# Kernel optimization log

Measured on AMD Instinct MI355X. Metric: run time of the kernel, lower is better.

## Reference

```python
import jax, jax.numpy as jnp
import numpy as np

EMB = 1024
HEADS = 16
RATE = 1.0


def setup_inputs() -> dict:
    key = jax.random.key(0)
    ks = jax.random.split(key, 11)
    B, S, D = 2, 2048, EMB
    s = 1.0 / np.sqrt(D)
    inp = {
        "q": jax.random.normal(ks[0], (B, S, D), jnp.float32),
        "k": jax.random.normal(ks[1], (B, S, D), jnp.float32),
        "v": jax.random.normal(ks[2], (B, S, D), jnp.float32),
        "Wq": jax.random.normal(ks[3], (D, D), jnp.float32) * s,
        "bq": jnp.zeros((D,), jnp.float32),
        "Wk": jax.random.normal(ks[4], (D, D), jnp.float32) * s,
        "bk": jnp.zeros((D,), jnp.float32),
        "Wv": jax.random.normal(ks[5], (D, D), jnp.float32) * s,
        "bv": jnp.zeros((D,), jnp.float32),
        "Wo": jax.random.normal(ks[6], (D, D), jnp.float32) * s,
        "bo": jnp.zeros((D,), jnp.float32),
    }
    return inp


def _mha(q, k, v, Wq, bq, Wk, bk, Wv, bv, Wo, bo):
    B, S, D = q.shape
    H = HEADS
    hd = D // H
    temp = jnp.asarray(hd ** 0.5, q.dtype)

    def proj(x, W, b):
        # nn.Linear: x @ W.T + b, then Scaler: /rate
        y = (jnp.einsum('bsd,ed->bse', x, W) + b) / RATE
        # [B,S,D] -> [B,H,S,hd]
        return y.reshape(B, S, H, hd).transpose(0, 2, 1, 3)

    qh, kh, vh = proj(q, Wq, bq), proj(k, Wk, bk), proj(v, Wv, bv)
    scores = jnp.einsum('bhqd,bhkd->bhqk', qh, kh) / temp  # [B,H,S,S]
    causal = jnp.tril(jnp.ones((S, S), bool))
    scores = jnp.where(causal, scores, jnp.asarray(-jnp.inf, scores.dtype))
    attn = jax.nn.softmax(scores, axis=-1)
    out = jnp.einsum('bhqk,bhkd->bhqd', attn, vh)  # [B,H,S,hd]
    out = out.transpose(0, 2, 1, 3).reshape(B, S, D)
    out = (jnp.einsum('bsd,ed->bse', out, Wo) + bo) / RATE
    # attn returned as [B*H, S, S] to match torch reshape-to-batches layout
    return out, attn.reshape(B * H, S, S)


def reference(q, k, v, Wq, bq, Wk, bk, Wv, bv, Wo, bo):
    return _mha(q, k, v, Wq, bq, Wk, bk, Wv, bv, Wo, bo)
```

## Files before the change

### kernel.cpp

```cpp
#include <hip/hip_runtime.h>
#include <hip/hip_bf16.h>
#include <stdint.h>


#define SLEN 2048
#define DMODEL 1024
#define NBH 32

typedef __bf16 bf16x8 __attribute__((ext_vector_type(8)));
typedef float f32x4 __attribute__((ext_vector_type(4)));
typedef unsigned short us8 __attribute__((ext_vector_type(8)));

__device__ __forceinline__ unsigned short f2bf(float f) {
  union { float f; uint32_t u; } x; x.f = f;
  uint32_t r = x.u + 0x7fffu + ((x.u >> 16) & 1u);
  return (unsigned short)(r >> 16);
}

__device__ __forceinline__ f32x4 mfma16(us8 a, us8 b, f32x4 c) {
  return __builtin_amdgcn_mfma_f32_16x16x32_bf16(
      __builtin_bit_cast(bf16x8, a), __builtin_bit_cast(bf16x8, b), c, 0, 0, 0);
}

__device__ __forceinline__ int sw8(int r, int c)  { return (r * 8  + (c ^ (r & 7)))  * 16; }
__device__ __forceinline__ int sw16(int r, int c) { return (r * 16 + (c ^ (r & 15))) * 16; }

__global__ __launch_bounds__(256)
void gemm_qkv(const float* __restrict__ xq, const float* __restrict__ xk,
              const float* __restrict__ xv, const float* __restrict__ wwq,
              const float* __restrict__ wwk, const float* __restrict__ wwv,
              const float* __restrict__ bbq, const float* __restrict__ bbk,
              const float* __restrict__ bbv,
              unsigned short* __restrict__ qh, unsigned short* __restrict__ kk,
              unsigned short* __restrict__ vt) {
  __shared__ __align__(16) unsigned char As[16384];
  __shared__ __align__(16) unsigned char Bs[16384];
  const int p = blockIdx.z;
  const float* X    = (p == 0) ? xq  : (p == 1) ? xk  : xv;
  const float* W    = (p == 0) ? wwq : (p == 1) ? wwk : wwv;
  const float* bias = (p == 0) ? bbq : (p == 1) ? bbk : bbv;
  const int n0 = blockIdx.x * 128, m0 = blockIdx.y * 128;
  const int t = threadIdx.x, lane = t & 63, w = t >> 6;
  const int quad = lane >> 4, l16 = lane & 15;
  const int wm = w >> 1, wn = w & 1;
  f32x4 acc[4][4] = {};

  for (int kt = 0; kt < 16; ++kt) {
#pragma unroll
    for (int i = 0; i < 4; ++i) {
      int lin = i * 256 + t;
      int r = lin >> 3, cp = lin & 7, c = cp ^ (r & 7);
      const float* g = X + (size_t)(m0 + r) * DMODEL + kt * 64 + c * 8;
      float4 f0 = *(const float4*)g;
      float4 f1 = *(const float4*)(g + 4);
      us8 u;
      u[0]=f2bf(f0.x); u[1]=f2bf(f0.y); u[2]=f2bf(f0.z); u[3]=f2bf(f0.w);
      u[4]=f2bf(f1.x); u[5]=f2bf(f1.y); u[6]=f2bf(f1.z); u[7]=f2bf(f1.w);
      *(us8*)(As + lin * 16) = u;
      const float* g2 = W + (size_t)(n0 + r) * DMODEL + kt * 64 + c * 8;
      float4 h0 = *(const float4*)g2;
      float4 h1 = *(const float4*)(g2 + 4);
      us8 vv;
      vv[0]=f2bf(h0.x); vv[1]=f2bf(h0.y); vv[2]=f2bf(h0.z); vv[3]=f2bf(h0.w);
      vv[4]=f2bf(h1.x); vv[5]=f2bf(h1.y); vv[6]=f2bf(h1.z); vv[7]=f2bf(h1.w);
      *(us8*)(Bs + lin * 16) = vv;
    }
    __syncthreads();
#pragma unroll
    for (int ks = 0; ks < 2; ++ks) {
      int c = ks * 4 + quad;
      us8 af[4], bf[4];
#pragma unroll
      for (int mt = 0; mt < 4; ++mt) af[mt] = *(const us8*)(As + sw8(wm * 64 + mt * 16 + l16, c));
#pragma unroll
      for (int nt = 0; nt < 4; ++nt) bf[nt] = *(const us8*)(Bs + sw8(wn * 64 + nt * 16 + l16, c));
#pragma unroll
      for (int mt = 0; mt < 4; ++mt)
#pragma unroll
        for (int nt = 0; nt < 4; ++nt)
          acc[mt][nt] = mfma16(af[mt], bf[nt], acc[mt][nt]);
    }
    __syncthreads();
  }
#pragma unroll
  for (int nt = 0; nt < 4; ++nt) {
    int e = n0 + wn * 64 + nt * 16 + l16;
    float bb = bias[e];
    int hh = e >> 6, tt = e & 63;
#pragma unroll
    for (int mt = 0; mt < 4; ++mt) {
#pragma unroll
      for (int rg = 0; rg < 4; ++rg) {
        int row = m0 + wm * 64 + mt * 16 + quad * 4 + rg;
        int b = row >> 11, s = row & 2047;
        unsigned short val = f2bf(acc[mt][nt][rg] + bb);
        int bhh = b * 16 + hh;
        if (p == 0)      qh[(size_t)(bhh * 2048 + s) * 64 + tt] = val;
        else if (p == 1) kk[(size_t)(bhh * 2048 + s) * 64 + tt] = val;
        else             vt[(size_t)(bhh * 64 + tt) * 2048 + s] = val;
      }
    }
  }
}

__global__ __launch_bounds__(256)
void attn_kernel(const unsigned short* __restrict__ qh,
                 const unsigned short* __restrict__ kk,
                 const unsigned short* __restrict__ vt,
                 unsigned short* __restrict__ ctx,
                 float* __restrict__ attn) {
  __shared__ __align__(16) unsigned char Ks[16384];
  __shared__ __align__(16) unsigned char Vts[16384];
  __shared__ __align__(16) unsigned char Ps[16384];
  const int bid = blockIdx.x;
  const int bh = bid >> 4;
  const int qt = (bid < 256) ? (bid & 15) : (15 - (bid & 15));
  const int q0 = qt * 128;
  const int t = threadIdx.x, lane = t & 63, w = t >> 6;
  const int quad = lane >> 4, l16 = lane & 15;
  const size_t bho = (size_t)bh * SLEN * 64;

  us8 qf[2][2];
#pragma unroll
  for (int mq = 0; mq < 2; ++mq)
#pragma unroll
    for (int ks = 0; ks < 2; ++ks)
      qf[mq][ks] = *(const us8*)(qh + bho + (size_t)(q0 + w * 32 + mq * 16 + l16) * 64 + ks * 32 + quad * 8);

  float mrow[2][4], lrow[2][4];
#pragma unroll
  for (int mq = 0; mq < 2; ++mq)
#pragma unroll
    for (int rg = 0; rg < 4; ++rg) { mrow[mq][rg] = -3e38f; lrow[mq][rg] = 0.f; }

  for (int kt = 0; kt <= qt; ++kt) {
    __syncthreads();
#pragma unroll
    for (int i = 0; i < 4; ++i) {
      int lin = i * 256 + t, r = lin >> 3, cp = lin & 7, c = cp ^ (r & 7);
      *(us8*)(Ks + lin * 16) = *(const us8*)(kk + bho + (size_t)(kt * 128 + r) * 64 + c * 8);
    }
    __syncthreads();
    f32x4 sacc[2][8] = {};
#pragma unroll
    for (int ks = 0; ks < 2; ++ks) {
      int c = ks * 4 + quad;
      us8 bfr[8];
#pragma unroll
      for (int nk = 0; nk < 8; ++nk) bfr[nk] = *(const us8*)(Ks + sw8(nk * 16 + l16, c));
#pragma unroll
      for (int mq = 0; mq < 2; ++mq)
#pragma unroll
        for (int nk = 0; nk < 8; ++nk)
          sacc[mq][nk] = mfma16(qf[mq][ks], bfr[nk], sacc[mq][nk]);
    }
    const bool diag = (kt == qt);
#pragma unroll
    for (int mq = 0; mq < 2; ++mq)
#pragma unroll
      for (int rg = 0; rg < 4; ++rg) {
        int qrow = q0 + w * 32 + mq * 16 + quad * 4 + rg;
        float sv[8];
        float pm = -3e38f;
#pragma unroll
        for (int nk = 0; nk < 8; ++nk) {
          float vvv = sacc[mq][nk][rg] * 0.125f;
          if (diag && (kt * 128 + nk * 16 + l16) > qrow) vvv = -3e38f;
          sv[nk] = vvv;
          pm = fmaxf(pm, vvv);
        }
        pm = fmaxf(pm, __shfl_xor(pm, 1));
        pm = fmaxf(pm, __shfl_xor(pm, 2));
        pm = fmaxf(pm, __shfl_xor(pm, 4));
        pm = fmaxf(pm, __shfl_xor(pm, 8));
        float mn = fmaxf(mrow[mq][rg], pm);
        float ps = 0.f;
#pragma unroll
        for (int nk = 0; nk < 8; ++nk) ps += __expf(sv[nk] - mn);
        ps += __shfl_xor(ps, 1);
        ps += __shfl_xor(ps, 2);
        ps += __shfl_xor(ps, 4);
        ps += __shfl_xor(ps, 8);
        lrow[mq][rg] = lrow[mq][rg] * __expf(mrow[mq][rg] - mn) + ps;
        mrow[mq][rg] = mn;
      }
  }
  float rl[2][4];
#pragma unroll
  for (int mq = 0; mq < 2; ++mq)
#pragma unroll
    for (int rg = 0; rg < 4; ++rg) rl[mq][rg] = 1.0f / lrow[mq][rg];

  f32x4 oacc[2][4] = {};
  float* attnb = attn + (size_t)bh * SLEN * SLEN + (size_t)q0 * SLEN;
  for (int kt = 0; kt < 16; ++kt) {
    if (kt <= qt) {
      __syncthreads();
#pragma unroll
      for (int i = 0; i < 4; ++i) {
        int lin = i * 256 + t, r = lin >> 3, cp = lin & 7, c = cp ^ (r & 7);
        *(us8*)(Ks + lin * 16) = *(const us8*)(kk + bho + (size_t)(kt * 128 + r) * 64 + c * 8);
      }
#pragma unroll
      for (int i = 0; i < 4; ++i) {
        int lin = i * 256 + t, r = lin >> 4, cp = lin & 15, c = cp ^ (r & 15);
        *(us8*)(Vts + lin * 16) = *(const us8*)(vt + bho + (size_t)r * SLEN + kt * 128 + c * 8);
      }
      __syncthreads();
      f32x4 sacc[2][8] = {};
#pragma unroll
      for (int ks = 0; ks < 2; ++ks) {
        int c = ks * 4 + quad;
        us8 bfr[8];
#pragma unroll
        for (int nk = 0; nk < 8; ++nk) bfr[nk] = *(const us8*)(Ks + sw8(nk * 16 + l16, c));
#pragma unroll
        for (int mq = 0; mq < 2; ++mq)
#pragma unroll
          for (int nk = 0; nk < 8; ++nk)
            sacc[mq][nk] = mfma16(qf[mq][ks], bfr[nk], sacc[mq][nk]);
      }
      const bool diag = (kt == qt);
#pragma unroll
      for (int mq = 0; mq < 2; ++mq)
#pragma unroll
        for (int nk = 0; nk < 8; ++nk) {
          int col = kt * 128 + nk * 16 + l16;
#pragma unroll
          for (int rg = 0; rg < 4; ++rg) {
            int qrow = q0 + w * 32 + mq * 16 + quad * 4 + rg;
            float vvv = sacc[mq][nk][rg] * 0.125f;
            float p = __expf(vvv - mrow[mq][rg]) * rl[mq][rg];
            if (diag && col > qrow) p = 0.f;
            sacc[mq][nk][rg] = p;
            attnb[(size_t)(w * 32 + mq * 16 + quad * 4 + rg) * SLEN + col] = p;
          }
        }
#pragma unroll
      for (int kh2 = 0; kh2 < 2; ++kh2) {
#pragma unroll
        for (int mq = 0; mq < 2; ++mq)
#pragma unroll
          for (int nkk = 0; nkk < 4; ++nkk) {
            int nk = kh2 * 4 + nkk;
#pragma unroll
            for (int rg = 0; rg < 4; ++rg) {
              int pr = w * 32 + mq * 16 + quad * 4 + rg;
              int kl = nkk * 16 + l16;
              *(unsigned short*)(Ps + (pr * 8 + ((kl >> 3) ^ (pr & 7))) * 16 + (kl & 7) * 2)
                  = f2bf(sacc[mq][nk][rg]);
            }
          }
#pragma unroll
        for (int ks = 0; ks < 2; ++ks) {
          int ca = ks * 4 + quad;
          us8 pa[2];
#pragma unroll
          for (int mq = 0; mq < 2; ++mq)
            pa[mq] = *(const us8*)(Ps + sw8(w * 32 + mq * 16 + l16, ca));
          int cb = kh2 * 8 + ks * 4 + quad;
          us8 vb[4];
#pragma unroll
          for (int nd = 0; nd < 4; ++nd) vb[nd] = *(const us8*)(Vts + sw16(nd * 16 + l16, cb));
#pragma unroll
          for (int mq = 0; mq < 2; ++mq)
#pragma unroll
            for (int nd = 0; nd < 4; ++nd)
              oacc[mq][nd] = mfma16(pa[mq], vb[nd], oacc[mq][nd]);
        }
      }
    } else {
      float4 z = make_float4(0.f, 0.f, 0.f, 0.f);
#pragma unroll
      for (int i = 0; i < 16; ++i) {
        int idx = i * 256 + t, r = idx >> 5, c4 = idx & 31;
        *(float4*)(attnb + (size_t)r * SLEN + kt * 128 + c4 * 4) = z;
      }
    }
  }
  int b = bh >> 4, h = bh & 15;
#pragma unroll
  for (int mq = 0; mq < 2; ++mq)
#pragma unroll
    for (int nd = 0; nd < 4; ++nd)
#pragma unroll
      for (int rg = 0; rg < 4; ++rg) {
        int qrow = q0 + w * 32 + mq * 16 + quad * 4 + rg;
        int e = h * 64 + nd * 16 + l16;
        ctx[(size_t)(b * SLEN + qrow) * DMODEL + e] = f2bf(oacc[mq][nd][rg]);
      }
}

__global__ __launch_bounds__(256)
void gemm_out(const unsigned short* __restrict__ ctx, const float* __restrict__ wo,
              const float* __restrict__ bo, float* __restrict__ out) {
  __shared__ __align__(16) unsigned char As[16384];
  __shared__ __align__(16) unsigned char Bs[16384];
  const int n0 = blockIdx.x * 128, m0 = blockIdx.y * 128;
  const int t = threadIdx.x, lane = t & 63, w = t >> 6;
  const int quad = lane >> 4, l16 = lane & 15;
  const int wm = w >> 1, wn = w & 1;
  f32x4 acc[4][4] = {};

  for (int kt = 0; kt < 16; ++kt) {
#pragma unroll
    for (int i = 0; i < 4; ++i) {
      int lin = i * 256 + t;
      int r = lin >> 3, cp = lin & 7, c = cp ^ (r & 7);
      *(us8*)(As + lin * 16) = *(const us8*)(ctx + (size_t)(m0 + r) * DMODEL + kt * 64 + c * 8);
      const float* g2 = wo + (size_t)(n0 + r) * DMODEL + kt * 64 + c * 8;
      float4 h0 = *(const float4*)g2;
      float4 h1 = *(const float4*)(g2 + 4);
      us8 vv;
      vv[0]=f2bf(h0.x); vv[1]=f2bf(h0.y); vv[2]=f2bf(h0.z); vv[3]=f2bf(h0.w);
      vv[4]=f2bf(h1.x); vv[5]=f2bf(h1.y); vv[6]=f2bf(h1.z); vv[7]=f2bf(h1.w);
      *(us8*)(Bs + lin * 16) = vv;
    }
    __syncthreads();
#pragma unroll
    for (int ks = 0; ks < 2; ++ks) {
      int c = ks * 4 + quad;
      us8 af[4], bf[4];
#pragma unroll
      for (int mt = 0; mt < 4; ++mt) af[mt] = *(const us8*)(As + sw8(wm * 64 + mt * 16 + l16, c));
#pragma unroll
      for (int nt = 0; nt < 4; ++nt) bf[nt] = *(const us8*)(Bs + sw8(wn * 64 + nt * 16 + l16, c));
#pragma unroll
      for (int mt = 0; mt < 4; ++mt)
#pragma unroll
        for (int nt = 0; nt < 4; ++nt)
          acc[mt][nt] = mfma16(af[mt], bf[nt], acc[mt][nt]);
    }
    __syncthreads();
  }
#pragma unroll
  for (int nt = 0; nt < 4; ++nt) {
    int e = n0 + wn * 64 + nt * 16 + l16;
    float bb = bo[e];
#pragma unroll
    for (int mt = 0; mt < 4; ++mt)
#pragma unroll
      for (int rg = 0; rg < 4; ++rg) {
        int row = m0 + wm * 64 + mt * 16 + quad * 4 + rg;
        out[(size_t)row * DMODEL + e] = acc[mt][nt][rg] + bb;
      }
  }
}

extern "C" void kernel_launch(void* const* d_in, const int* in_sizes, int n_in,
                              void* d_out, int out_size, void* d_ws, size_t ws_size,
                              hipStream_t stream) {
  const float* q  = (const float*)d_in[0];
  const float* k  = (const float*)d_in[1];
  const float* v  = (const float*)d_in[2];
  const float* Wq = (const float*)d_in[3];
  const float* bq = (const float*)d_in[4];
  const float* Wk = (const float*)d_in[5];
  const float* bk = (const float*)d_in[6];
  const float* Wv = (const float*)d_in[7];
  const float* bv = (const float*)d_in[8];
  const float* Wo = (const float*)d_in[9];
  const float* bo = (const float*)d_in[10];
  float* out  = (float*)d_out;
  float* attn = out + (size_t)2 * SLEN * DMODEL;

  unsigned short* qh  = (unsigned short*)d_ws;
  unsigned short* kh  = qh + (size_t)4194304;
  unsigned short* vt  = kh + (size_t)4194304;
  unsigned short* ctx = vt + (size_t)4194304;

  gemm_qkv<<<dim3(8, 32, 3), 256, 0, stream>>>(q, k, v, Wq, Wk, Wv, bq, bk, bv, qh, kh, vt);
  attn_kernel<<<512, 256, 0, stream>>>(qh, kh, vt, ctx, attn);
  gemm_out<<<dim3(8, 32), 256, 0, stream>>>(ctx, Wo, bo, out);
}
```

Measured before the change: 874.2 us.

## Pre-convert inputs to bf16 and use direct global-to-LDS loads

Result: faster. 794.0 us (-9.2%).

```diff
diff --git a/kernel.cpp b/kernel.cpp
--- a/kernel.cpp
+++ b/kernel.cpp
@@ -22,17 +22,112 @@
       __builtin_bit_cast(bf16x8, a), __builtin_bit_cast(bf16x8, b), c, 0, 0, 0);
 }
 
+__device__ __forceinline__ void gld16(void* lds, const void* g) {
+  __builtin_amdgcn_global_load_lds(
+      (__attribute__((address_space(1))) void*)(g),
+      (__attribute__((address_space(3))) void*)(lds), 16, 0, 0);
+}
+
 __device__ __forceinline__ int sw8(int r, int c)  { return (r * 8  + (c ^ (r & 7)))  * 16; }
 __device__ __forceinline__ int sw16(int r, int c) { return (r * 16 + (c ^ (r & 15))) * 16; }
 
 __global__ __launch_bounds__(256)
-void gemm_qkv(const float* __restrict__ xq, const float* __restrict__ xk,
-              const float* __restrict__ xv, const float* __restrict__ wwq,
-              const float* __restrict__ wwk, const float* __restrict__ wwv,
-              const float* __restrict__ bbq, const float* __restrict__ bbk,
-              const float* __restrict__ bbv,
-              unsigned short* __restrict__ qh, unsigned short* __restrict__ kk,
-              unsigned short* __restrict__ vt) {
+void convert_bf16(const float* __restrict__ q, const float* __restrict__ k,
+                  const float* __restrict__ v, const float* __restrict__ wq,
+                  const float* __restrict__ wk, const float* __restrict__ wv,
+                  const float* __restrict__ wo, unsigned short* __restrict__ dst) {
+  size_t i = ((size_t)blockIdx.x * 256 + threadIdx.x) * 8;
+  const float* src;
+  size_t off;
+  if      (i <  4194304u) { src = q;  off = i; }
+  else if (i <  8388608u) { src = k;  off = i -  4194304u; }
+  else if (i < 12582912u) { src = v;  off = i -  8388608u; }
+  else if (i < 13631488u) { src = wq; off = i - 12582912u; }
+  else if (i < 14680064u) { src = wk; off = i - 13631488u; }
+  else if (i < 15728640u) { src = wv; off = i - 14680064u; }
+  else                    { src = wo; off = i - 15728640u; }
+  float4 a = *(const float4*)(src + off);
+  float4 b = *(const float4*)(src + off + 4);
+  us8 u;
+  u[0]=f2bf(a.x); u[1]=f2bf(a.y); u[2]=f2bf(a.z); u[3]=f2bf(a.w);
+  u[4]=f2bf(b.x); u[5]=f2bf(b.y); u[6]=f2bf(b.z); u[7]=f2bf(b.w);
+  *(us8*)(dst + i) = u;
+}
+
+__global__ __launch_bounds__(256)
+void gemm_qkv_bf(const unsigned short* __restrict__ xq, const unsigned short* __restrict__ xk,
+                 const unsigned short* __restrict__ xv, const unsigned short* __restrict__ wwq,
+                 const unsigned short* __restrict__ wwk, const unsigned short* __restrict__ wwv,
+                 const float* __restrict__ bbq, const float* __restrict__ bbk,
+                 const float* __restrict__ bbv,
+                 unsigned short* __restrict__ qh, unsigned short* __restrict__ kk,
+                 unsigned short* __restrict__ vt) {
+  __shared__ __align__(16) unsigned char As[16384];
+  __shared__ __align__(16) unsigned char Bs[16384];
+  const int p = blockIdx.z;
+  const unsigned short* X = (p == 0) ? xq  : (p == 1) ? xk  : xv;
+  const unsigned short* W = (p == 0) ? wwq : (p == 1) ? wwk : wwv;
+  const float* bias       = (p == 0) ? bbq : (p == 1) ? bbk : bbv;
+  const int n0 = blockIdx.x * 128, m0 = blockIdx.y * 128;
+  const int t = threadIdx.x, lane = t & 63, w = t >> 6;
+  const int quad = lane >> 4, l16 = lane & 15;
+  const int wm = w >> 1, wn = w & 1;
+  f32x4 acc[4][4] = {};
+
+  for (int kt = 0; kt < 16; ++kt) {
+#pragma unroll
+    for (int i = 0; i < 4; ++i) {
+      int lin = i * 256 + t;
+      int r = lin >> 3, cp = lin & 7, c = cp ^ (r & 7);
+      gld16(As + lin * 16, X + (size_t)(m0 + r) * DMODEL + kt * 64 + c * 8);
+      gld16(Bs + lin * 16, W + (size_t)(n0 + r) * DMODEL + kt * 64 + c * 8);
+    }
+    __syncthreads();
+#pragma unroll
+    for (int ks = 0; ks < 2; ++ks) {
+      int c = ks * 4 + quad;
+      us8 af[4], bf[4];
+#pragma unroll
+      for (int mt = 0; mt < 4; ++mt) af[mt] = *(const us8*)(As + sw8(wm * 64 + mt * 16 + l16, c));
+#pragma unroll
+      for (int nt = 0; nt < 4; ++nt) bf[nt] = *(const us8*)(Bs + sw8(wn * 64 + nt * 16 + l16, c));
+#pragma unroll
+      for (int mt = 0; mt < 4; ++mt)
+#pragma unroll
+        for (int nt = 0; nt < 4; ++nt)
+          acc[mt][nt] = mfma16(af[mt], bf[nt], acc[mt][nt]);
+    }
+    __syncthreads();
+  }
+#pragma unroll
+  for (int nt = 0; nt < 4; ++nt) {
+    int e = n0 + wn * 64 + nt * 16 + l16;
+    float bb = bias[e];
+    int hh = e >> 6, tt = e & 63;
+#pragma unroll
+    for (int mt = 0; mt < 4; ++mt) {
+#pragma unroll
+      for (int rg = 0; rg < 4; ++rg) {
+        int row = m0 + wm * 64 + mt * 16 + quad * 4 + rg;
+        int b = row >> 11, s = row & 2047;
+        unsigned short val = f2bf(acc[mt][nt][rg] + bb);
+        int bhh = b * 16 + hh;
+        if (p == 0)      qh[(size_t)(bhh * 2048 + s) * 64 + tt] = val;
+        else if (p == 1) kk[(size_t)(bhh * 2048 + s) * 64 + tt] = val;
+        else             vt[(size_t)(bhh * 64 + tt) * 2048 + s] = val;
+      }
+    }
+  }
+}
+
+__global__ __launch_bounds__(256)
+void gemm_qkv_f32(const float* __restrict__ xq, const float* __restrict__ xk,
+                  const float* __restrict__ xv, const float* __restrict__ wwq,
+                  const float* __restrict__ wwk, const float* __restrict__ wwv,
+                  const float* __restrict__ bbq, const float* __restrict__ bbk,
+                  const float* __restrict__ bbv,
+                  unsigned short* __restrict__ qh, unsigned short* __restrict__ kk,
+                  unsigned short* __restrict__ vt) {
   __shared__ __align__(16) unsigned char As[16384];
   __shared__ __align__(16) unsigned char Bs[16384];
   const int p = blockIdx.z;
@@ -138,7 +233,7 @@
 #pragma unroll
     for (int i = 0; i < 4; ++i) {
       int lin = i * 256 + t, r = lin >> 3, cp = lin & 7, c = cp ^ (r & 7);
-      *(us8*)(Ks + lin * 16) = *(const us8*)(kk + bho + (size_t)(kt * 128 + r) * 64 + c * 8);
+      gld16(Ks + lin * 16, kk + bho + (size_t)(kt * 128 + r) * 64 + c * 8);
     }
     __syncthreads();
     f32x4 sacc[2][8] = {};
@@ -199,12 +294,12 @@
 #pragma unroll
       for (int i = 0; i < 4; ++i) {
         int lin = i * 256 + t, r = lin >> 3, cp = lin & 7, c = cp ^ (r & 7);
-        *(us8*)(Ks + lin * 16) = *(const us8*)(kk + bho + (size_t)(kt * 128 + r) * 64 + c * 8);
+        gld16(Ks + lin * 16, kk + bho + (size_t)(kt * 128 + r) * 64 + c * 8);
       }
 #pragma unroll
       for (int i = 0; i < 4; ++i) {
         int lin = i * 256 + t, r = lin >> 4, cp = lin & 15, c = cp ^ (r & 15);
-        *(us8*)(Vts + lin * 16) = *(const us8*)(vt + bho + (size_t)r * SLEN + kt * 128 + c * 8);
+        gld16(Vts + lin * 16, vt + bho + (size_t)r * SLEN + kt * 128 + c * 8);
       }
       __syncthreads();
       f32x4 sacc[2][8] = {};
@@ -292,8 +387,8 @@
 }
 
 __global__ __launch_bounds__(256)
-void gemm_out(const unsigned short* __restrict__ ctx, const float* __restrict__ wo,
-              const float* __restrict__ bo, float* __restrict__ out) {
+void gemm_out_bf(const unsigned short* __restrict__ ctx, const unsigned short* __restrict__ wo,
+                 const float* __restrict__ bo, float* __restrict__ out) {
   __shared__ __align__(16) unsigned char As[16384];
   __shared__ __align__(16) unsigned char Bs[16384];
   const int n0 = blockIdx.x * 128, m0 = blockIdx.y * 128;
@@ -307,7 +402,57 @@
     for (int i = 0; i < 4; ++i) {
       int lin = i * 256 + t;
       int r = lin >> 3, cp = lin & 7, c = cp ^ (r & 7);
-      *(us8*)(As + lin * 16) = *(const us8*)(ctx + (size_t)(m0 + r) * DMODEL + kt * 64 + c * 8);
+      gld16(As + lin * 16, ctx + (size_t)(m0 + r) * DMODEL + kt * 64 + c * 8);
+      gld16(Bs + lin * 16, wo  + (size_t)(n0 + r) * DMODEL + kt * 64 + c * 8);
+    }
+    __syncthreads();
+#pragma unroll
+    for (int ks = 0; ks < 2; ++ks) {
+      int c = ks * 4 + quad;
+      us8 af[4], bf[4];
+#pragma unroll
+      for (int mt = 0; mt < 4; ++mt) af[mt] = *(const us8*)(As + sw8(wm * 64 + mt * 16 + l16, c));
+#pragma unroll
+      for (int nt = 0; nt < 4; ++nt) bf[nt] = *(const us8*)(Bs + sw8(wn * 64 + nt * 16 + l16, c));
+#pragma unroll
+      for (int mt = 0; mt < 4; ++mt)
+#pragma unroll
+        for (int nt = 0; nt < 4; ++nt)
+          acc[mt][nt] = mfma16(af[mt], bf[nt], acc[mt][nt]);
+    }
+    __syncthreads();
+  }
+#pragma unroll
+  for (int nt = 0; nt < 4; ++nt) {
+    int e = n0 + wn * 64 + nt * 16 + l16;
+    float bb = bo[e];
+#pragma unroll
+    for (int mt = 0; mt < 4; ++mt)
+#pragma unroll
+      for (int rg = 0; rg < 4; ++rg) {
+        int row = m0 + wm * 64 + mt * 16 + quad * 4 + rg;
+        out[(size_t)row * DMODEL + e] = acc[mt][nt][rg] + bb;
+      }
+  }
+}
+
+__global__ __launch_bounds__(256)
+void gemm_out_f32(const unsigned short* __restrict__ ctx, const float* __restrict__ wo,
+                  const float* __restrict__ bo, float* __restrict__ out) {
+  __shared__ __align__(16) unsigned char As[16384];
+  __shared__ __align__(16) unsigned char Bs[16384];
+  const int n0 = blockIdx.x * 128, m0 = blockIdx.y * 128;
+  const int t = threadIdx.x, lane = t & 63, w = t >> 6;
+  const int quad = lane >> 4, l16 = lane & 15;
+  const int wm = w >> 1, wn = w & 1;
+  f32x4 acc[4][4] = {};
+
+  for (int kt = 0; kt < 16; ++kt) {
+#pragma unroll
+    for (int i = 0; i < 4; ++i) {
+      int lin = i * 256 + t;
+      int r = lin >> 3, cp = lin & 7, c = cp ^ (r & 7);
+      gld16(As + lin * 16, ctx + (size_t)(m0 + r) * DMODEL + kt * 64 + c * 8);
       const float* g2 = wo + (size_t)(n0 + r) * DMODEL + kt * 64 + c * 8;
       float4 h0 = *(const float4*)g2;
       float4 h1 = *(const float4*)(g2 + 4);
@@ -365,11 +510,29 @@
   float* attn = out + (size_t)2 * SLEN * DMODEL;
 
   unsigned short* qh  = (unsigned short*)d_ws;
-  unsigned short* kh  = qh + (size_t)4194304;
-  unsigned short* vt  = kh + (size_t)4194304;
-  unsigned short* ctx = vt + (size_t)4194304;
-
-  gemm_qkv<<<dim3(8, 32, 3), 256, 0, stream>>>(q, k, v, Wq, Wk, Wv, bq, bk, bv, qh, kh, vt);
-  attn_kernel<<<512, 256, 0, stream>>>(qh, kh, vt, ctx, attn);
-  gemm_out<<<dim3(8, 32), 256, 0, stream>>>(ctx, Wo, bo, out);
-}
+  unsigned short* kh  = qh  + (size_t)4194304;
+  unsigned short* vt  = kh  + (size_t)4194304;
+  unsigned short* ctx = vt  + (size_t)4194304;
+  unsigned short* xbq = ctx + (size_t)4194304;
+  unsigned short* xbk = xbq + (size_t)4194304;
+  unsigned short* xbv = xbk + (size_t)4194304;
+  unsigned short* wbq = xbv + (size_t)4194304;
+  unsigned short* wbk = wbq + (size_t)1048576;
+  unsigned short* wbv = wbk + (size_t)1048576;
+  unsigned short* wbo = wbv + (size_t)1048576;
+
+  const size_t WS_FULL = (size_t)67108864;
+
+  if (ws_size >= WS_FULL) {
+    convert_bf16<<<8192, 256, 0, stream>>>(q, k, v, Wq, Wk, Wv, Wo, xbq);
+    gemm_qkv_bf<<<dim3(8, 32, 3), 256, 0, stream>>>(xbq, xbk, xbv, wbq, wbk, wbv,
+                                                    bq, bk, bv, qh, kh, vt);
+    attn_kernel<<<512, 256, 0, stream>>>(qh, kh, vt, ctx, attn);
+    gemm_out_bf<<<dim3(8, 32), 256, 0, stream>>>(ctx, wbo, bo, out);
+  } else {
+    gemm_qkv_f32<<<dim3(8, 32, 3), 256, 0, stream>>>(q, k, v, Wq, Wk, Wv,
+                                                     bq, bk, bv, qh, kh, vt);
+    attn_kernel<<<512, 256, 0, stream>>>(qh, kh, vt, ctx, attn);
+    gemm_out_f32<<<dim3(8, 32), 256, 0, stream>>>(ctx, Wo, bo, out);
+  }
+}
```
